# Optimization experiments

Measured on AMD Instinct MI355X. Metric: run time of the kernel, lower is better.

## Reference

```python
import jax, jax.numpy as jnp
import numpy as np

OUT_FEATURES = 4096
IN_FEATURES = 4096
GROUP_SIZE = 128
NUMEL = OUT_FEATURES * IN_FEATURES  # 16777216


def setup_inputs() -> dict:
    key = jax.random.key(0)
    k1, k2, k3, k4, k5 = jax.random.split(key, 5)
    x = jax.random.normal(k1, (4, 2048, IN_FEATURES), dtype=jnp.float32)
    # two int4 values packed per byte -> NUMEL // 2 bytes
    packed = jax.random.randint(k2, (NUMEL // 2,), 0, 256, dtype=jnp.int32)
    # per-group scale/offset (NUMEL // GROUP_SIZE groups)
    scales = jax.random.uniform(k3, (NUMEL // GROUP_SIZE,), dtype=jnp.float32) * 0.1 + 1e-3
    offsets = jax.random.normal(k4, (NUMEL // GROUP_SIZE,), dtype=jnp.float32) * 0.01
    bias = jax.random.normal(k5, (OUT_FEATURES,), dtype=jnp.float32)
    return {"x": x, "packed": packed, "scales": scales, "offsets": offsets, "bias": bias}


def int4_dequantize(packed, scales, offsets):
    # low nibble, then high nibble, interleaved: [l0, h0, l1, h1, ...]
    low = packed & 15
    high = (packed >> 4) & 15
    q = jnp.stack([low, high], axis=1).reshape(-1).astype(jnp.float32)  # [NUMEL]
    groups = q.reshape(-1, GROUP_SIZE)  # [n_groups, group_size]
    w = groups * scales[:, None] + offsets[:, None]
    return w.reshape(OUT_FEATURES, IN_FEATURES)


def reference(x, packed, scales, offsets, bias):
    w = int4_dequantize(packed, scales, offsets)  # [out, in]
    # F.linear: y = x @ w.T + bias
    return jnp.einsum('bsi,oi->bso', x, w) + bias
```

## Files before the change

kernel.cpp:

```cpp
#include <hip/hip_runtime.h>
#include <stdint.h>

typedef __attribute__((ext_vector_type(4))) float  f32x4;
typedef __attribute__((ext_vector_type(4))) int    i32x4;
typedef __attribute__((ext_vector_type(8))) __bf16 bf16x8;

constexpr int M_DIM = 8192, N_DIM = 4096, K_DIM = 4096;

#define VMCNT(n) asm volatile("s_waitcnt vmcnt(" #n ")" ::: "memory")
#define LGKMCNT0 asm volatile("s_waitcnt lgkmcnt(0)" ::: "memory")

__global__ __launch_bounds__(256) void cvt_x(const float* __restrict__ X,
                                             __bf16* __restrict__ Xb) {
  size_t i = ((size_t)blockIdx.x * 256 + threadIdx.x) * 8;
  const f32x4* src = (const f32x4*)(X + i);
  f32x4 a = src[0], b = src[1];
  bf16x8 v;
  v[0] = (__bf16)a[0]; v[1] = (__bf16)a[1]; v[2] = (__bf16)a[2]; v[3] = (__bf16)a[3];
  v[4] = (__bf16)b[0]; v[5] = (__bf16)b[1]; v[6] = (__bf16)b[2]; v[7] = (__bf16)b[3];
  *(bf16x8*)(Xb + i) = v;
}

__global__ __launch_bounds__(256) void deq_w(const int* __restrict__ P,
                                             const float* __restrict__ S,
                                             const float* __restrict__ O,
                                             __bf16* __restrict__ Wb) {
  size_t i = (size_t)blockIdx.x * 256 + threadIdx.x;
  const i32x4* src = (const i32x4*)(P + i * 16);
  int g = (int)(i >> 2);
  float s = S[g], o = O[g];
  __bf16* dst = Wb + i * 32;
#pragma unroll
  for (int j = 0; j < 4; ++j) {
    i32x4 p = src[j];
    bf16x8 v;
#pragma unroll
    for (int b = 0; b < 4; ++b) {
      int pv = p[b];
      v[2 * b]     = (__bf16)fmaf((float)(pv & 15), s, o);
      v[2 * b + 1] = (__bf16)fmaf((float)((pv >> 4) & 15), s, o);
    }
    *(bf16x8*)(dst + j * 8) = v;
  }
}

__device__ __forceinline__ void stage64(const char* g, size_t rs, char* l, int tid) {
  const int r = tid >> 3;
  const int c = ((tid & 7) * 16) ^ ((r & 7) << 4);
  __builtin_amdgcn_global_load_lds(
      (const __attribute__((address_space(1))) uint32_t*)(g + (size_t)r * rs + c),
      (__attribute__((address_space(3))) uint32_t*)(l + (tid >> 6) * 1024),
      16, 0, 0);
}

__global__ __launch_bounds__(512, 2) void gemm8(const __bf16* __restrict__ A,
                                                const __bf16* __restrict__ B,
                                                const float* __restrict__ Bias,
                                                float* __restrict__ Y) {
  extern __shared__ char lds[];

  constexpr int NT = K_DIM / 64;
  const int tid  = threadIdx.x;
  const int lane = tid & 63;
  const int wid  = tid >> 6;
  const int wm   = wid >> 2;
  const int wn   = wid & 3;
  const int ln15 = lane & 15;
  const int lq   = lane >> 4;

  const int id  = blockIdx.y * gridDim.x + blockIdx.x;
  const int swz = (id & 7) * 64 + (id >> 3);
  const int bn0 = (swz & 15) * 256;
  const int bm0 = (swz >> 4) * 256;

  const size_t rs = (size_t)K_DIM * 2;
  const char* Ag = (const char*)A + (size_t)bm0 * rs;
  const char* Bg = (const char*)B + (size_t)bn0 * rs;

  f32x4 acc[8][4];
#pragma unroll
  for (int m = 0; m < 8; ++m)
#pragma unroll
    for (int n = 0; n < 4; ++n)
      acc[m][n] = (f32x4){0.f, 0.f, 0.f, 0.f};

  {
    char* Ab = lds;
    char* Bb = lds + 65536;
    stage64(Bg + (size_t)0 * rs,   rs, Bb + 0,     tid);
    stage64(Bg + (size_t)64 * rs,  rs, Bb + 8192,  tid);
    stage64(Bg + (size_t)128 * rs, rs, Bb + 16384, tid);
    stage64(Bg + (size_t)192 * rs, rs, Bb + 24576, tid);
    stage64(Ag + (size_t)0 * rs,   rs, Ab + 0,     tid);
    stage64(Ag + (size_t)128 * rs, rs, Ab + 16384, tid);
    stage64(Ag + (size_t)64 * rs,  rs, Ab + 8192,  tid);
    stage64(Ag + (size_t)192 * rs, rs, Ab + 24576, tid);
  }
  VMCNT(2);
  __builtin_amdgcn_s_barrier();

  for (int t = 0; t < NT; ++t) {
    const char* Ab = lds + (t & 1) * 32768;
    const char* Bb = lds + 65536 + (t & 1) * 32768;
    char* An = lds + ((t + 1) & 1) * 32768;
    char* Bn = lds + 65536 + ((t + 1) & 1) * 32768;
    const bool st = (t + 1 < NT);
    const char* ga = Ag + (size_t)(t + 1) * 128;
    const char* gb = Bg + (size_t)(t + 1) * 128;

    bf16x8 bfr[4];

#pragma unroll
    for (int q = 0; q < 4; ++q) {
      const int mh = q & 1, ks = q >> 1;
      __builtin_amdgcn_sched_barrier(0);

      if (mh == 0) {
#pragma unroll
        for (int n = 0; n < 4; ++n) {
          const int r  = wn * 64 + n * 16 + ln15;
          const int sw = (r & 7) << 4;
          bfr[n] = *(const bf16x8*)(Bb + r * 128 + ((ks * 64 + lq * 16) ^ sw));
        }
      }
      bf16x8 af[4];
#pragma unroll
      for (int m4 = 0; m4 < 4; ++m4) {
        const int r  = wm * 128 + (mh * 4 + m4) * 16 + ln15;
        const int sw = (r & 7) << 4;
        af[m4] = *(const bf16x8*)(Ab + r * 128 + ((ks * 64 + lq * 16) ^ sw));
      }

      if (st) {
        if (q == 0) { stage64(gb, rs, Bn, tid);
                      stage64(gb + (size_t)64 * rs, rs, Bn + 8192, tid); }
        if (q == 1) { stage64(gb + (size_t)128 * rs, rs, Bn + 16384, tid);
                      stage64(gb + (size_t)192 * rs, rs, Bn + 24576, tid); }
        if (q == 2) { stage64(ga, rs, An, tid);
                      stage64(ga + (size_t)128 * rs, rs, An + 16384, tid); }
        if (q == 3) { stage64(ga + (size_t)64 * rs, rs, An + 8192, tid);
                      stage64(ga + (size_t)192 * rs, rs, An + 24576, tid); }
      }

      __builtin_amdgcn_s_barrier();
      LGKMCNT0;
      __builtin_amdgcn_sched_barrier(0);

      __builtin_amdgcn_s_setprio(1);
#pragma unroll
      for (int m4 = 0; m4 < 4; ++m4)
#pragma unroll
        for (int n = 0; n < 4; ++n)
          acc[mh * 4 + m4][n] = __builtin_amdgcn_mfma_f32_16x16x32_bf16(
              af[m4], bfr[n], acc[mh * 4 + m4][n], 0, 0, 0);
      __builtin_amdgcn_s_setprio(0);
      __builtin_amdgcn_sched_barrier(0);

      if (q == 0) {
        if (t == NT - 1) { VMCNT(0); } else { VMCNT(2); }
      }
      if (q == 3 && st) { VMCNT(2); }
      __builtin_amdgcn_s_barrier();
    }
  }

#pragma unroll
  for (int n = 0; n < 4; ++n) {
    const int col = bn0 + wn * 64 + n * 16 + ln15;
    const float bias = Bias[col];
#pragma unroll
    for (int m = 0; m < 8; ++m) {
      const int row0 = bm0 + wm * 128 + m * 16 + lq * 4;
#pragma unroll
      for (int r = 0; r < 4; ++r)
        Y[(size_t)(row0 + r) * N_DIM + col] = acc[m][n][r] + bias;
    }
  }
}

__global__ __launch_bounds__(256) void qlin_fused_gemm(
    const float* __restrict__ X, const int* __restrict__ P,
    const float* __restrict__ S, const float* __restrict__ Ofs,
    const float* __restrict__ Bias, float* __restrict__ Y)
{
  constexpr int BM = 128, BN = 128, BK = 64;
  constexpr int NT = K_DIM / BK;
  __shared__ __bf16 As[BM * BK];
  __shared__ __bf16 Bs[BN * BK];

  const int tid  = threadIdx.x;
  const int lane = tid & 63;
  const int wv   = tid >> 6;
  const int wr   = (wv >> 1) * 64;
  const int wc   = (wv & 1) * 64;
  const int bn0 = blockIdx.x * BN;
  const int bm0 = blockIdx.y * BM;
  const int srow  = tid >> 1;
  const int shalf = tid & 1;

  const float* xrow = X + (size_t)(bm0 + srow) * K_DIM + shalf * 32;
  const int*   prow = P + (size_t)(bn0 + srow) * (K_DIM / 2) + shalf * 16;
  const int    gbase = (bn0 + srow) * (K_DIM / 128);

  const int rowb = srow * (BK * 2);
  const int sxor = (srow & 7) << 4;
  const int cbb  = shalf * 64;

  f32x4 areg[8];
  i32x4 breg[4];
  float sc, of;

  f32x4 acc[4][4];
#pragma unroll
  for (int i = 0; i < 4; ++i)
#pragma unroll
    for (int j = 0; j < 4; ++j)
      acc[i][j] = (f32x4){0.f, 0.f, 0.f, 0.f};

#pragma unroll
  for (int i = 0; i < 8; ++i) areg[i] = *(const f32x4*)(xrow + 4 * i);
#pragma unroll
  for (int i = 0; i < 4; ++i) breg[i] = *(const i32x4*)(prow + 4 * i);
  sc = S[gbase];
  of = Ofs[gbase];

  for (int kt = 0; kt < NT; ++kt) {
    __syncthreads();
    {
      char* ab = (char*)As + rowb;
      char* bb = (char*)Bs + rowb;
#pragma unroll
      for (int i = 0; i < 4; ++i) {
        bf16x8 v;
        f32x4 u0 = areg[2 * i], u1 = areg[2 * i + 1];
        v[0] = (__bf16)u0[0]; v[1] = (__bf16)u0[1];
        v[2] = (__bf16)u0[2]; v[3] = (__bf16)u0[3];
        v[4] = (__bf16)u1[0]; v[5] = (__bf16)u1[1];
        v[6] = (__bf16)u1[2]; v[7] = (__bf16)u1[3];
        *(bf16x8*)(ab + ((cbb + 16 * i) ^ sxor)) = v;
      }
#pragma unroll
      for (int i = 0; i < 4; ++i) {
        bf16x8 v;
        i32x4 p = breg[i];
#pragma unroll
        for (int j = 0; j < 4; ++j) {
          int pv = p[j];
          v[2 * j]     = (__bf16)fmaf((float)(pv & 15), sc, of);
          v[2 * j + 1] = (__bf16)fmaf((float)((pv >> 4) & 15), sc, of);
        }
        *(bf16x8*)(bb + ((cbb + 16 * i) ^ sxor)) = v;
      }
    }
    if (kt + 1 < NT) {
      const float* xp = xrow + (kt + 1) * BK;
#pragma unroll
      for (int i = 0; i < 8; ++i) areg[i] = *(const f32x4*)(xp + 4 * i);
      const int* pp = prow + (kt + 1) * (BK / 2);
#pragma unroll
      for (int i = 0; i < 4; ++i) breg[i] = *(const i32x4*)(pp + 4 * i);
      int g = gbase + (kt + 1) / 2;
      sc = S[g]; of = Ofs[g];
    }
    __syncthreads();
#pragma unroll
    for (int ks = 0; ks < 2; ++ks) {
      const int cb = ks * 64 + (lane >> 4) * 16;
      bf16x8 afr[4], bfr[4];
#pragma unroll
      for (int m = 0; m < 4; ++m) {
        int r = wr + m * 16 + (lane & 15);
        afr[m] = *(const bf16x8*)((const char*)As + r * (BK * 2) + (cb ^ ((r & 7) << 4)));
      }
#pragma unroll
      for (int n = 0; n < 4; ++n) {
        int r = wc + n * 16 + (lane & 15);
        bfr[n] = *(const bf16x8*)((const char*)Bs + r * (BK * 2) + (cb ^ ((r & 7) << 4)));
      }
#pragma unroll
      for (int m = 0; m < 4; ++m)
#pragma unroll
        for (int n = 0; n < 4; ++n)
          acc[m][n] = __builtin_amdgcn_mfma_f32_16x16x32_bf16(afr[m], bfr[n], acc[m][n], 0, 0, 0);
    }
  }
#pragma unroll
  for (int n = 0; n < 4; ++n) {
    const int col = bn0 + wc + n * 16 + (lane & 15);
    const float bias = Bias[col];
#pragma unroll
    for (int m = 0; m < 4; ++m) {
      const int row0 = bm0 + wr + m * 16 + (lane >> 4) * 4;
#pragma unroll
      for (int r = 0; r < 4; ++r)
        Y[(size_t)(row0 + r) * N_DIM + col] = acc[m][n][r] + bias;
    }
  }
}

extern "C" void kernel_launch(void* const* d_in, const int* in_sizes, int n_in,
                              void* d_out, int out_size, void* d_ws, size_t ws_size,
                              hipStream_t stream) {
  const float* X    = (const float*)d_in[0];
  const int*   P    = (const int*)d_in[1];
  const float* S    = (const float*)d_in[2];
  const float* Ofs  = (const float*)d_in[3];
  const float* Bias = (const float*)d_in[4];
  float* Y = (float*)d_out;

  const size_t xb_bytes = (size_t)M_DIM * K_DIM * 2;
  const size_t wb_bytes = (size_t)N_DIM * K_DIM * 2;

  if (ws_size >= xb_bytes + wb_bytes) {
    __bf16* Xb = (__bf16*)d_ws;
    __bf16* Wb = (__bf16*)((char*)d_ws + xb_bytes);

    cvt_x<<<dim3((M_DIM * K_DIM) / (256 * 8)), dim3(256), 0, stream>>>(X, Xb);
    deq_w<<<dim3((N_DIM * K_DIM) / (256 * 32)), dim3(256), 0, stream>>>(P, S, Ofs, Wb);

    hipFuncSetAttribute((const void*)gemm8,
                        hipFuncAttributeMaxDynamicSharedMemorySize, 131072);
    dim3 grid(N_DIM / 256, M_DIM / 256);
    gemm8<<<grid, dim3(512), 131072, stream>>>(Xb, Wb, Bias, Y);
  } else {
    dim3 grid(N_DIM / 128, M_DIM / 128);
    qlin_fused_gemm<<<grid, dim3(256), 0, stream>>>(X, P, S, Ofs, Bias, Y);
  }
}
```

Measured before the change: 275.4 us.

## Software-pipeline LDS fragment reads ahead of MFMA in bf16 GEMM main loop

Restructures the gemm8 K-loop so LDS fragment reads for the next quarter-step are issued before the barrier and overlap the current MFMA block, using double-buffered register fragments (af0/af1, bf0/bf1). It also issues part of the next B tile's global-to-LDS loads two iterations ahead, into the buffer half just consumed, and adjusts vmcnt waits accordingly. The aim is to hide LDS latency and global-load latency behind the matrix instructions. In exchange it uses more registers and relies on delicate vmcnt and barrier ordering, which risks races if the counts are off.

```diff
diff --git a/kernel.cpp b/kernel.cpp
--- a/kernel.cpp
+++ b/kernel.cpp
@@ -9,6 +9,7 @@
 
 #define VMCNT(n) asm volatile("s_waitcnt vmcnt(" #n ")" ::: "memory")
 #define LGKMCNT0 asm volatile("s_waitcnt lgkmcnt(0)" ::: "memory")
+#define SB __builtin_amdgcn_sched_barrier(0)
 
 __global__ __launch_bounds__(256) void cvt_x(const float* __restrict__ X,
                                              __bf16* __restrict__ Xb) {
@@ -53,6 +54,38 @@
       16, 0, 0);
 }
 
+__device__ __forceinline__ void read_a(bf16x8 (&dst)[4], const char* Ab,
+                                       int wm, int ln15, int lq, int mh, int ks) {
+#pragma unroll
+  for (int m4 = 0; m4 < 4; ++m4) {
+    const int r = wm * 128 + (mh * 4 + m4) * 16 + ln15;
+    const int sw = (r & 7) << 4;
+    dst[m4] = *(const bf16x8*)(Ab + r * 128 + ((ks * 64 + lq * 16) ^ sw));
+  }
+}
+
+__device__ __forceinline__ void read_b(bf16x8 (&dst)[4], const char* Bb,
+                                       int wn, int ln15, int lq, int ks) {
+#pragma unroll
+  for (int n = 0; n < 4; ++n) {
+    const int r = wn * 64 + n * 16 + ln15;
+    const int sw = (r & 7) << 4;
+    dst[n] = *(const bf16x8*)(Bb + r * 128 + ((ks * 64 + lq * 16) ^ sw));
+  }
+}
+
+__device__ __forceinline__ void mfma16(f32x4 (&acc)[8][4], const bf16x8 (&af)[4],
+                                       const bf16x8 (&bf)[4], int mbase) {
+  __builtin_amdgcn_s_setprio(1);
+#pragma unroll
+  for (int m4 = 0; m4 < 4; ++m4)
+#pragma unroll
+    for (int n = 0; n < 4; ++n)
+      acc[mbase + m4][n] = __builtin_amdgcn_mfma_f32_16x16x32_bf16(
+          af[m4], bf[n], acc[mbase + m4][n], 0, 0, 0);
+  __builtin_amdgcn_s_setprio(0);
+}
+
 __global__ __launch_bounds__(512, 2) void gemm8(const __bf16* __restrict__ A,
                                                 const __bf16* __restrict__ B,
                                                 const float* __restrict__ Bias,
@@ -83,6 +116,8 @@
 #pragma unroll
     for (int n = 0; n < 4; ++n)
       acc[m][n] = (f32x4){0.f, 0.f, 0.f, 0.f};
+
+  bf16x8 af0[4], af1[4], bf0[4], bf1[4];
 
   {
     char* Ab = lds;
@@ -95,72 +130,74 @@
     stage64(Ag + (size_t)128 * rs, rs, Ab + 16384, tid);
     stage64(Ag + (size_t)64 * rs,  rs, Ab + 8192,  tid);
     stage64(Ag + (size_t)192 * rs, rs, Ab + 24576, tid);
-  }
-  VMCNT(2);
+    char* Bn = lds + 65536 + 32768;
+    stage64(Bg + 128,                 rs, Bn + 0,    tid);
+    stage64(Bg + (size_t)64 * rs + 128, rs, Bn + 8192, tid);
+  }
+  VMCNT(4);
+  SB;
   __builtin_amdgcn_s_barrier();
+  read_b(bf0, lds + 65536, wn, ln15, lq, 0);
+  read_a(af0, lds,         wm, ln15, lq, 0, 0);
 
   for (int t = 0; t < NT; ++t) {
     const char* Ab = lds + (t & 1) * 32768;
     const char* Bb = lds + 65536 + (t & 1) * 32768;
-    char* An = lds + ((t + 1) & 1) * 32768;
-    char* Bn = lds + 65536 + ((t + 1) & 1) * 32768;
-    const bool st = (t + 1 < NT);
-    const char* ga = Ag + (size_t)(t + 1) * 128;
-    const char* gb = Bg + (size_t)(t + 1) * 128;
-
-    bf16x8 bfr[4];
-
-#pragma unroll
-    for (int q = 0; q < 4; ++q) {
-      const int mh = q & 1, ks = q >> 1;
-      __builtin_amdgcn_sched_barrier(0);
-
-      if (mh == 0) {
-#pragma unroll
-        for (int n = 0; n < 4; ++n) {
-          const int r  = wn * 64 + n * 16 + ln15;
-          const int sw = (r & 7) << 4;
-          bfr[n] = *(const bf16x8*)(Bb + r * 128 + ((ks * 64 + lq * 16) ^ sw));
-        }
-      }
-      bf16x8 af[4];
-#pragma unroll
-      for (int m4 = 0; m4 < 4; ++m4) {
-        const int r  = wm * 128 + (mh * 4 + m4) * 16 + ln15;
-        const int sw = (r & 7) << 4;
-        af[m4] = *(const bf16x8*)(Ab + r * 128 + ((ks * 64 + lq * 16) ^ sw));
-      }
-
-      if (st) {
-        if (q == 0) { stage64(gb, rs, Bn, tid);
-                      stage64(gb + (size_t)64 * rs, rs, Bn + 8192, tid); }
-        if (q == 1) { stage64(gb + (size_t)128 * rs, rs, Bn + 16384, tid);
-                      stage64(gb + (size_t)192 * rs, rs, Bn + 24576, tid); }
-        if (q == 2) { stage64(ga, rs, An, tid);
-                      stage64(ga + (size_t)128 * rs, rs, An + 16384, tid); }
-        if (q == 3) { stage64(ga + (size_t)64 * rs, rs, An + 8192, tid);
-                      stage64(ga + (size_t)192 * rs, rs, An + 24576, tid); }
-      }
-
+    char* An  = lds + ((t + 1) & 1) * 32768;
+    char* Bn  = lds + 65536 + ((t + 1) & 1) * 32768;
+    char* Bn2 = lds + 65536 + (t & 1) * 32768;
+    const bool s1 = (t + 1 < NT);
+    const bool s2 = (t + 2 < NT);
+    const char* ga1 = Ag + (size_t)(t + 1) * 128;
+    const char* gb1 = Bg + (size_t)(t + 1) * 128;
+    const char* gb2 = Bg + (size_t)(t + 2) * 128;
+
+    LGKMCNT0; SB;
+    mfma16(acc, af0, bf0, 0);
+    SB;
+    if (s1) {
+      stage64(gb1 + (size_t)128 * rs, rs, Bn + 16384, tid);
+      stage64(gb1 + (size_t)192 * rs, rs, Bn + 24576, tid);
+      stage64(ga1,                    rs, An + 0,     tid);
+    }
+    if (t == NT - 1) { VMCNT(0); } else { VMCNT(5); }
+    SB;
+    __builtin_amdgcn_s_barrier();
+    read_a(af1, Ab, wm, ln15, lq, 1, 0);
+
+    LGKMCNT0; SB;
+    mfma16(acc, af1, bf0, 4);
+    SB;
+    if (s1) {
+      stage64(ga1 + (size_t)128 * rs, rs, An + 16384, tid);
+      stage64(ga1 + (size_t)64 * rs,  rs, An + 8192,  tid);
+      stage64(ga1 + (size_t)192 * rs, rs, An + 24576, tid);
+    }
+    read_b(bf1, Bb, wn, ln15, lq, 1);
+    read_a(af0, Ab, wm, ln15, lq, 0, 1);
+    SB;
+    __builtin_amdgcn_s_barrier();
+
+    LGKMCNT0; SB;
+    mfma16(acc, af0, bf1, 0);
+    SB;
+    read_a(af1, Ab, wm, ln15, lq, 1, 1);
+    SB;
+    __builtin_amdgcn_s_barrier();
+
+    LGKMCNT0; SB;
+    mfma16(acc, af1, bf1, 4);
+    SB;
+    if (s1) {
+      VMCNT(2);
+      SB;
       __builtin_amdgcn_s_barrier();
-      LGKMCNT0;
-      __builtin_amdgcn_sched_barrier(0);
-
-      __builtin_amdgcn_s_setprio(1);
-#pragma unroll
-      for (int m4 = 0; m4 < 4; ++m4)
-#pragma unroll
-        for (int n = 0; n < 4; ++n)
-          acc[mh * 4 + m4][n] = __builtin_amdgcn_mfma_f32_16x16x32_bf16(
-              af[m4], bfr[n], acc[mh * 4 + m4][n], 0, 0, 0);
-      __builtin_amdgcn_s_setprio(0);
-      __builtin_amdgcn_sched_barrier(0);
-
-      if (q == 0) {
-        if (t == NT - 1) { VMCNT(0); } else { VMCNT(2); }
-      }
-      if (q == 3 && st) { VMCNT(2); }
-      __builtin_amdgcn_s_barrier();
+      if (s2) {
+        stage64(gb2,                   rs, Bn2 + 0,    tid);
+        stage64(gb2 + (size_t)64 * rs, rs, Bn2 + 8192, tid);
+      }
+      read_b(bf0, Bn, wn, ln15, lq, 0);
+      read_a(af0, An, wm, ln15, lq, 0, 0);
     }
   }
 
```

Result: faster. 268.4 us (-2.5%).
